# Kernel tuning notes

Measured on AMD Instinct MI355X. Metric: run time of the kernel, lower is better.

## Reference

```python
import jax, jax.numpy as jnp
import numpy as np

B, L, D = 8, 1024, 512
NB = 4              # num_blocks
DIN = 2 * D         # mamba expand=2
N = 16              # d_state
DTR = 32            # dt_rank = ceil(D/16)
DCONV = 4           # mamba depthwise conv kernel
FF = 2 * D          # ffn_expand=2
EPS = 1e-5


def setup_inputs() -> dict:
    key = jax.random.key(0)
    ks = iter(jax.random.split(key, 64))

    def rnd(shape, s=0.02):
        return jax.random.normal(next(ks), shape, jnp.float32) * s

    p = {}
    p["x"] = jax.random.normal(next(ks), (B, L, D), jnp.float32)
    # TemporalConvBlock (Conv1d D->D, k=3, pad=1, groups=1) + LayerNorm
    p["tconv_w"] = rnd((D, D, 3), 0.05)
    p["tconv_b"] = jnp.zeros((D,), jnp.float32)
    p["tnorm_w"] = jnp.ones((D,), jnp.float32)
    p["tnorm_b"] = jnp.zeros((D,), jnp.float32)
    # per-block params, stacked on leading NB axis
    p["ln1_w"] = jnp.ones((NB, D), jnp.float32)
    p["ln1_b"] = jnp.zeros((NB, D), jnp.float32)
    p["in_proj_w"] = rnd((NB, 2 * DIN, D))          # no bias (mamba default)
    p["conv_w"] = rnd((NB, DIN, 1, DCONV), 0.1)     # depthwise causal conv
    p["conv_b"] = jnp.zeros((NB, DIN), jnp.float32)
    p["x_proj_w"] = rnd((NB, DTR + 2 * N, DIN))     # no bias
    p["dt_proj_w"] = rnd((NB, DIN, DTR), 0.1)
    p["dt_proj_b"] = jnp.log(jnp.expm1(jnp.full((NB, DIN), 0.01, jnp.float32)))
    p["A_log"] = jnp.tile(jnp.log(jnp.arange(1, N + 1, dtype=jnp.float32))[None, None, :], (NB, DIN, 1))
    p["D_param"] = jnp.ones((NB, DIN), jnp.float32)
    p["out_proj_w"] = rnd((NB, D, DIN))             # no bias
    p["ln2_w"] = jnp.ones((NB, D), jnp.float32)
    p["ln2_b"] = jnp.zeros((NB, D), jnp.float32)
    p["ffn_w1"] = rnd((NB, FF, D))
    p["ffn_b1"] = jnp.zeros((NB, FF), jnp.float32)
    p["ffn_w2"] = rnd((NB, D, FF))
    p["ffn_b2"] = jnp.zeros((NB, D), jnp.float32)
    return p


def _ln(x, w, b):
    mu = jnp.mean(x, -1, keepdims=True)
    v = jnp.mean(jnp.square(x - mu), -1, keepdims=True)
    return (x - mu) * jax.lax.rsqrt(v + EPS) * w + b


def _selective_scan(u, dt, A, Bm, C, Dp):
    # u, dt: (B,L,DIN); A: (DIN,N); Bm, C: (B,L,N); Dp: (DIN,)
    def step(h, inp):
        u_t, dt_t, B_t, C_t = inp                      # (B,DIN),(B,DIN),(B,N),(B,N)
        dA = jnp.exp(dt_t[..., None] * A)              # (B,DIN,N)
        dBu = dt_t[..., None] * B_t[:, None, :] * u_t[..., None]
        h = dA * h + dBu
        y = jnp.einsum('bdn,bn->bd', h, C_t)
        return h, y

    h0 = jnp.zeros((u.shape[0], A.shape[0], A.shape[1]), u.dtype)
    xs = (u.swapaxes(0, 1), dt.swapaxes(0, 1), Bm.swapaxes(0, 1), C.swapaxes(0, 1))
    _, ys = jax.lax.scan(step, h0, xs)                 # ys: (L,B,DIN)
    return ys.swapaxes(0, 1) + u * Dp


def _mamba(x, in_w, cw, cb, xpw, dtw, dtb, A_log, Dp, ow):
    xz = jnp.einsum('bld,ed->ble', x, in_w)            # (B,L,2*DIN)
    u, z = jnp.split(xz, 2, axis=-1)
    # causal depthwise conv over time
    uc = u.swapaxes(1, 2)                              # (B,DIN,L)
    uc = jax.lax.conv_general_dilated(
        uc, cw, (1,), [(DCONV - 1, 0)],
        feature_group_count=DIN, dimension_numbers=('NCH', 'OIH', 'NCH'))
    uc = uc + cb[None, :, None]
    u = jax.nn.silu(uc.swapaxes(1, 2))                 # (B,L,DIN)
    xdb = jnp.einsum('bld,ed->ble', u, xpw)            # (B,L,DTR+2N)
    dtr, Bm, C = jnp.split(xdb, [DTR, DTR + N], axis=-1)
    dt = jax.nn.softplus(jnp.einsum('blr,dr->bld', dtr, dtw) + dtb)
    A = -jnp.exp(A_log)
    y = _selective_scan(u, dt, A, Bm, C, Dp)
    y = y * jax.nn.silu(z)
    return jnp.einsum('bld,ed->ble', y, ow)


def reference(x, tconv_w, tconv_b, tnorm_w, tnorm_b, ln1_w, ln1_b, in_proj_w,
              conv_w, conv_b, x_proj_w, dt_proj_w, dt_proj_b, A_log, D_param,
              out_proj_w, ln2_w, ln2_b, ffn_w1, ffn_b1, ffn_w2, ffn_b2):
    # TemporalConvBlock (dropout = identity in eval)
    hc = jax.lax.conv_general_dilated(
        x.swapaxes(1, 2), tconv_w, (1,), [(1, 1)],
        dimension_numbers=('NCH', 'OIH', 'NCH'))
    hc = (hc + tconv_b[None, :, None]).swapaxes(1, 2)
    h = _ln(hc + x, tnorm_w, tnorm_b)
    # stacked MambaWithFFN blocks
    for i in range(NB):
        h = h + _mamba(_ln(h, ln1_w[i], ln1_b[i]), in_proj_w[i], conv_w[i],
                       conv_b[i], x_proj_w[i], dt_proj_w[i], dt_proj_b[i],
                       A_log[i], D_param[i], out_proj_w[i])
        hn = _ln(h, ln2_w[i], ln2_b[i])
        ff = jax.nn.gelu(jnp.einsum('bld,fd->blf', hn, ffn_w1[i]) + ffn_b1[i],
                         approximate=False)
        h = h + jnp.einsum('blf,df->bld', ff, ffn_w2[i]) + ffn_b2[i]
    return h
```

## Files before the change

kernel.cpp:

```cpp
#include <hip/hip_runtime.h>
#include <hip/hip_bf16.h>
#include <math.h>

#define B_ 8
#define L_ 1024
#define D_ 512
#define NB_ 4
#define DIN_ 1024
#define NST_ 16
#define DTR_ 32
#define FF_ 1024
#define EPS_LN 1e-5f
#define M_ (B_ * L_)

#define SC_G 16
#define SC_C 32
#define SC_LEN (L_ / SC_C)

typedef __attribute__((ext_vector_type(8))) short short8;
typedef __attribute__((ext_vector_type(4))) float f32x4;

static __device__ __forceinline__ ushort f2bf(float f) {
  union { float f; unsigned u; } v; v.f = f;
  unsigned r = v.u + 0x7FFFu + ((v.u >> 16) & 1u);
  return (ushort)(r >> 16);
}
static __device__ __forceinline__ float bf2f(ushort u) {
  union { unsigned u; float f; } v; v.u = ((unsigned)u) << 16;
  return v.f;
}

template <int MODE, int EPI, int BN, int AF32, int OUTB>
__global__ __launch_bounds__(256) void mgemm_k(
    const void* __restrict__ Ap, const ushort* __restrict__ W,
    const float* __restrict__ bias, void* __restrict__ Cp,
    float* __restrict__ C2, int M, int N, int K, int lda, int ldc)
{
  constexpr int FN = BN / 32;
  __shared__ ushort As[128 * 32];
  __shared__ ushort Bs[BN * 32];
  const int tid = threadIdx.x;
  const int lane = tid & 63;
  const int wid = tid >> 6;
  const int wm = (wid >> 1) * 64;
  const int wn = (wid & 1) * (BN / 2);
  const int bm = blockIdx.y * 128;
  const int bn = blockIdx.x * BN;
  const int fr = lane & 15;
  const int kq = lane >> 4;

  f32x4 acc[4][FN];
#pragma unroll
  for (int i = 0; i < 4; ++i)
#pragma unroll
    for (int j = 0; j < FN; ++j) acc[i][j] = (f32x4)0.f;

  for (int k0 = 0; k0 < K; k0 += 32) {
#pragma unroll
    for (int it = 0; it < 2; ++it) {
      const int idx = tid + it * 256;
      const int row = idx >> 2;
      const int j = idx & 3;
      short8 s;
      if (AF32) {
        float4 v0, v1;
        if (MODE == 0) {
          const float* p = (const float*)Ap + (size_t)(bm + row) * lda + k0 + j * 8;
          v0 = *(const float4*)p; v1 = *(const float4*)(p + 4);
        } else {
          const int kk = k0 + j * 8;
          const int tap = kk >> 9;
          const int dcol = kk & 511;
          const int m = bm + row;
          const int l = (m & (L_ - 1)) + tap - 1;
          if (l >= 0 && l < L_) {
            const float* p = (const float*)Ap + (size_t)(m - (m & (L_ - 1)) + l) * D_ + dcol;
            v0 = *(const float4*)p; v1 = *(const float4*)(p + 4);
          } else {
            v0 = make_float4(0.f, 0.f, 0.f, 0.f); v1 = v0;
          }
        }
        s[0] = (short)f2bf(v0.x); s[1] = (short)f2bf(v0.y);
        s[2] = (short)f2bf(v0.z); s[3] = (short)f2bf(v0.w);
        s[4] = (short)f2bf(v1.x); s[5] = (short)f2bf(v1.y);
        s[6] = (short)f2bf(v1.z); s[7] = (short)f2bf(v1.w);
      } else {
        s = *(const short8*)((const ushort*)Ap + (size_t)(bm + row) * lda + k0 + j * 8);
      }
      *(short8*)&As[row * 32 + ((j ^ ((row >> 1) & 3)) << 3)] = s;
    }
#pragma unroll
    for (int it = 0; it < BN / 64; ++it) {
      const int idx = tid + it * 256;
      const int row = idx >> 2;
      const int j = idx & 3;
      short8 s = *(const short8*)(W + (size_t)(bn + row) * K + k0 + j * 8);
      *(short8*)&Bs[row * 32 + ((j ^ ((row >> 1) & 3)) << 3)] = s;
    }
    __syncthreads();
    short8 af[4], bfr[FN];
#pragma unroll
    for (int mi = 0; mi < 4; ++mi) {
      const int r = wm + mi * 16 + fr;
      af[mi] = *(const short8*)&As[r * 32 + ((kq ^ ((r >> 1) & 3)) << 3)];
    }
#pragma unroll
    for (int ni = 0; ni < FN; ++ni) {
      const int r = wn + ni * 16 + fr;
      bfr[ni] = *(const short8*)&Bs[r * 32 + ((kq ^ ((r >> 1) & 3)) << 3)];
    }
#pragma unroll
    for (int mi = 0; mi < 4; ++mi)
#pragma unroll
      for (int ni = 0; ni < FN; ++ni)
        acc[mi][ni] = __builtin_amdgcn_mfma_f32_16x16x32_bf16(
            af[mi], bfr[ni], acc[mi][ni], 0, 0, 0);
    __syncthreads();
  }

#pragma unroll
  for (int mi = 0; mi < 4; ++mi) {
#pragma unroll
    for (int ni = 0; ni < FN; ++ni) {
#pragma unroll
      for (int r = 0; r < 4; ++r) {
        const int gm = bm + wm + mi * 16 + (lane >> 4) * 4 + r;
        const int gn = bn + wn + ni * 16 + fr;
        float v = acc[mi][ni][r];
        if (EPI == 6) {
          if (gn < DIN_) {
            v += bias[gn];
            v = (v > 20.f) ? v : log1pf(__expf(v));
            ((float*)Cp)[(size_t)gm * DIN_ + gn] = v;
          } else if (gn < DIN_ + 2 * NST_) {
            C2[(size_t)gm * (2 * NST_) + (gn - DIN_)] = v;
          }
        } else {
          if (EPI == 1 || EPI == 2 || EPI == 3 || EPI == 5) v += bias[gn];
          if (EPI == 2) v = 0.5f * v * (1.f + erff(v * 0.70710678118654752f));
          if (EPI == 3) v = (v > 20.f) ? v : log1pf(__expf(v));
          if (OUTB) {
            ((ushort*)Cp)[(size_t)gm * ldc + gn] = f2bf(v);
          } else {
            float* pc = (float*)Cp + (size_t)gm * ldc + gn;
            if (EPI == 4 || EPI == 5) v += *pc;
            *pc = v;
          }
        }
      }
    }
  }
}

template <int INB, int OUTB>
__global__ __launch_bounds__(256) void ln_k(
    const void* __restrict__ inp, const float* __restrict__ res,
    const float* __restrict__ w, const float* __restrict__ b,
    void* __restrict__ outp)
{
  const int row = blockIdx.x;
  const int t = threadIdx.x;
  float v0, v1;
  if (INB) {
    const ushort* p = (const ushort*)inp + (size_t)row * D_;
    v0 = bf2f(p[t]); v1 = bf2f(p[t + 256]);
  } else {
    const float* p = (const float*)inp + (size_t)row * D_;
    v0 = p[t]; v1 = p[t + 256];
  }
  if (res) {
    const float* r = res + (size_t)row * D_;
    v0 += r[t]; v1 += r[t + 256];
  }
  float s = v0 + v1;
  float sq = v0 * v0 + v1 * v1;
#pragma unroll
  for (int m = 1; m < 64; m <<= 1) {
    s += __shfl_xor(s, m, 64);
    sq += __shfl_xor(sq, m, 64);
  }
  __shared__ float ss[4], qq[4];
  const int wid = t >> 6;
  if ((t & 63) == 0) { ss[wid] = s; qq[wid] = sq; }
  __syncthreads();
  s = ss[0] + ss[1] + ss[2] + ss[3];
  sq = qq[0] + qq[1] + qq[2] + qq[3];
  const float mu = s * (1.f / (float)D_);
  const float var = sq * (1.f / (float)D_) - mu * mu;
  const float rs = rsqrtf(var + EPS_LN);
  const float o0 = (v0 - mu) * rs * w[t] + b[t];
  const float o1 = (v1 - mu) * rs * w[t + 256] + b[t + 256];
  if (OUTB) {
    ushort* o = (ushort*)outp + (size_t)row * D_;
    o[t] = f2bf(o0); o[t + 256] = f2bf(o1);
  } else {
    float* o = (float*)outp + (size_t)row * D_;
    o[t] = o0; o[t + 256] = o1;
  }
}

__global__ __launch_bounds__(256) void dwconv_k(
    const ushort* __restrict__ xz, const float* __restrict__ cw,
    const float* __restrict__ cb, ushort* __restrict__ u)
{
  const int idx = blockIdx.x * 256 + threadIdx.x;
  const int c8 = idx & (DIN_ / 8 - 1);
  const int bl = idx >> 7;
  const int l = bl & (L_ - 1);
  const int b0 = bl - l;
  const int c0 = c8 * 8;
  float s[8], w[8][4];
#pragma unroll
  for (int j = 0; j < 8; ++j) {
    s[j] = cb[c0 + j];
    const float4 wv = *(const float4*)(cw + (c0 + j) * 4);
    w[j][0] = wv.x; w[j][1] = wv.y; w[j][2] = wv.z; w[j][3] = wv.w;
  }
#pragma unroll
  for (int k = 0; k < 4; ++k) {
    const int ll = l + k - 3;
    if (ll >= 0) {
      const short8 v = *(const short8*)(xz + (size_t)(b0 + ll) * (2 * DIN_) + c0);
#pragma unroll
      for (int j = 0; j < 8; ++j)
        s[j] = fmaf(bf2f((ushort)v[j]), w[j][k], s[j]);
    }
  }
  short8 o;
#pragma unroll
  for (int j = 0; j < 8; ++j) {
    const float t = s[j] / (1.f + __expf(-s[j]));
    o[j] = (short)f2bf(t);
  }
  *(short8*)(u + (size_t)idx * 8) = o;
}

template <bool FAST>
static __device__ __forceinline__ void dAcalc(float dtv, float A0,
                                              const float* A, float* dA)
{
  if (FAST) {
    const float e = __expf(dtv * A0);
    dA[0] = e;
#pragma unroll
    for (int n = 1; n < 16; ++n) dA[n] = dA[n - 1] * e;
  } else {
#pragma unroll
    for (int n = 0; n < 16; ++n) dA[n] = __expf(dtv * A[n]);
  }
}

template <bool FAST>
static __device__ __forceinline__ void scan_run(
    const float* __restrict__ dt, ushort* __restrict__ u,
    const float* __restrict__ BC, const ushort* __restrict__ xz,
    const float* __restrict__ A_log,
    const float* A, const float A0, const float Dpd,
    float (*Hs)[SC_G][NST_ + 1], float (*Ss)[SC_G],
    const int tid, const int g, const int c, const int d0, const int d,
    const size_t base)
{
  const int l0 = c * SC_LEN;
  float h[16];
#pragma unroll
  for (int n = 0; n < 16; ++n) h[n] = 0.f;
  float S = 0.f;

  {
    size_t row = base + l0;
    float dtv = dt[row * DIN_ + d];
    float uv = bf2f(u[row * DIN_ + d]);
    float Bv[16];
    *(float4*)&Bv[0]  = *(const float4*)(BC + row * 32);
    *(float4*)&Bv[4]  = *(const float4*)(BC + row * 32 + 4);
    *(float4*)&Bv[8]  = *(const float4*)(BC + row * 32 + 8);
    *(float4*)&Bv[12] = *(const float4*)(BC + row * 32 + 12);
    for (int i = 0; i < SC_LEN; ++i) {
      float ndt = 0.f, nu = 0.f;
      float NBv[16];
      if (i + 1 < SC_LEN) {
        const size_t nrow = row + 1;
        ndt = dt[nrow * DIN_ + d];
        nu = bf2f(u[nrow * DIN_ + d]);
        *(float4*)&NBv[0]  = *(const float4*)(BC + nrow * 32);
        *(float4*)&NBv[4]  = *(const float4*)(BC + nrow * 32 + 4);
        *(float4*)&NBv[8]  = *(const float4*)(BC + nrow * 32 + 8);
        *(float4*)&NBv[12] = *(const float4*)(BC + nrow * 32 + 12);
      }
      S += dtv;
      const float du = dtv * uv;
      float dA[16];
      dAcalc<FAST>(dtv, A0, A, dA);
#pragma unroll
      for (int n = 0; n < 16; ++n)
        h[n] = fmaf(dA[n], h[n], du * Bv[n]);
      dtv = ndt; uv = nu;
#pragma unroll
      for (int n = 0; n < 16; ++n) Bv[n] = NBv[n];
      row += 1;
    }
  }
#pragma unroll
  for (int n = 0; n < 16; ++n) Hs[c][g][n] = h[n];
  Ss[c][g] = S;
  __syncthreads();

  if (tid < SC_G * NST_) {
    const int gg = tid >> 4;
    const int n2 = tid & 15;
    const float An = -expf(A_log[(d0 + gg) * NST_ + n2]);
    float hin = 0.f;
#pragma unroll
    for (int cc = 0; cc < SC_C; ++cc) {
      const float tmp = Hs[cc][gg][n2];
      const float P = __expf(An * Ss[cc][gg]);
      Hs[cc][gg][n2] = hin;
      hin = tmp + P * hin;
    }
  }
  __syncthreads();

#pragma unroll
  for (int n = 0; n < 16; ++n) h[n] = Hs[c][g][n];
  {
    size_t row = base + l0;
    float dtv = dt[row * DIN_ + d];
    float uv = bf2f(u[row * DIN_ + d]);
    float zv = bf2f(xz[row * (2 * DIN_) + DIN_ + d]);
    float Bv[16], Cv[16];
    *(float4*)&Bv[0]  = *(const float4*)(BC + row * 32);
    *(float4*)&Bv[4]  = *(const float4*)(BC + row * 32 + 4);
    *(float4*)&Bv[8]  = *(const float4*)(BC + row * 32 + 8);
    *(float4*)&Bv[12] = *(const float4*)(BC + row * 32 + 12);
    *(float4*)&Cv[0]  = *(const float4*)(BC + row * 32 + 16);
    *(float4*)&Cv[4]  = *(const float4*)(BC + row * 32 + 20);
    *(float4*)&Cv[8]  = *(const float4*)(BC + row * 32 + 24);
    *(float4*)&Cv[12] = *(const float4*)(BC + row * 32 + 28);
    for (int i = 0; i < SC_LEN; ++i) {
      float ndt = 0.f, nu = 0.f, nz = 0.f;
      float NBv[16], NCv[16];
      if (i + 1 < SC_LEN) {
        const size_t nrow = row + 1;
        ndt = dt[nrow * DIN_ + d];
        nu = bf2f(u[nrow * DIN_ + d]);
        nz = bf2f(xz[nrow * (2 * DIN_) + DIN_ + d]);
        *(float4*)&NBv[0]  = *(const float4*)(BC + nrow * 32);
        *(float4*)&NBv[4]  = *(const float4*)(BC + nrow * 32 + 4);
        *(float4*)&NBv[8]  = *(const float4*)(BC + nrow * 32 + 8);
        *(float4*)&NBv[12] = *(const float4*)(BC + nrow * 32 + 12);
        *(float4*)&NCv[0]  = *(const float4*)(BC + nrow * 32 + 16);
        *(float4*)&NCv[4]  = *(const float4*)(BC + nrow * 32 + 20);
        *(float4*)&NCv[8]  = *(const float4*)(BC + nrow * 32 + 24);
        *(float4*)&NCv[12] = *(const float4*)(BC + nrow * 32 + 28);
      }
      const float du = dtv * uv;
      float y = uv * Dpd;
      float dA[16];
      dAcalc<FAST>(dtv, A0, A, dA);
#pragma unroll
      for (int n = 0; n < 16; ++n) {
        h[n] = fmaf(dA[n], h[n], du * Bv[n]);
        y = fmaf(h[n], Cv[n], y);
      }
      y *= zv / (1.f + __expf(-zv));
      u[row * DIN_ + d] = f2bf(y);
      dtv = ndt; uv = nu; zv = nz;
#pragma unroll
      for (int n = 0; n < 16; ++n) { Bv[n] = NBv[n]; Cv[n] = NCv[n]; }
      row += 1;
    }
  }
}

__global__ __launch_bounds__(512) void scan5_k(
    const float* __restrict__ dt, ushort* u,
    const float* __restrict__ BC, const ushort* __restrict__ xz,
    const float* __restrict__ A_log, const float* __restrict__ Dp)
{
  const int tid = threadIdx.x;
  const int g = tid & (SC_G - 1);
  const int c = tid >> 4;
  const int b = blockIdx.x >> 6;
  const int d0 = (blockIdx.x & 63) * SC_G;
  const int d = d0 + g;

  __shared__ float Hs[SC_C][SC_G][NST_ + 1];
  __shared__ float Ss[SC_C][SC_G];
  __shared__ int slow;
  if (tid == 0) slow = 0;
  __syncthreads();

  float A[16];
#pragma unroll
  for (int n = 0; n < 16; ++n) A[n] = -expf(A_log[d * NST_ + n]);
  const float A0 = A[0];
  bool myfast = true;
#pragma unroll
  for (int n = 1; n < 16; ++n)
    myfast = myfast && (fabsf(A[n] - (float)(n + 1) * A0) <= 1e-3f * fabsf(A[n]));
  if (!myfast) slow = 1;
  __syncthreads();
  const float Dpd = Dp[d];
  const size_t base = (size_t)b * L_;

  if (slow == 0)
    scan_run<true>(dt, u, BC, xz, A_log, A, A0, Dpd, Hs, Ss, tid, g, c, d0, d, base);
  else
    scan_run<false>(dt, u, BC, xz, A_log, A, A0, Dpd, Hs, Ss, tid, g, c, d0, d, base);
}

__global__ __launch_bounds__(256) void cvt_k(const float* __restrict__ in,
                                             ushort* __restrict__ out, int n8)
{
  const int i = blockIdx.x * 256 + threadIdx.x;
  if (i >= n8) return;
  const float4 a = *(const float4*)(in + (size_t)i * 8);
  const float4 b = *(const float4*)(in + (size_t)i * 8 + 4);
  short8 s;
  s[0] = (short)f2bf(a.x); s[1] = (short)f2bf(a.y);
  s[2] = (short)f2bf(a.z); s[3] = (short)f2bf(a.w);
  s[4] = (short)f2bf(b.x); s[5] = (short)f2bf(b.y);
  s[6] = (short)f2bf(b.z); s[7] = (short)f2bf(b.w);
  *(short8*)(out + (size_t)i * 8) = s;
}

__global__ __launch_bounds__(256) void twt_k(const float* __restrict__ in,
                                             ushort* __restrict__ out)
{
  const int i = blockIdx.x * 256 + threadIdx.x;
  if (i >= D_ * D_ * 3) return;
  const int o = i / (D_ * 3);
  const int rem = i - o * (D_ * 3);
  const int d = rem / 3;
  const int tap = rem - d * 3;
  out[(size_t)o * (D_ * 3) + tap * D_ + d] = f2bf(in[i]);
}

__global__ __launch_bounds__(256) void xpT_k(const float* __restrict__ xpw,
                                             ushort* __restrict__ out)
{
  const int i = blockIdx.x * 256 + threadIdx.x;
  if (i >= DIN_ * DTR_) return;
  const int k = i >> 5;
  const int r = i & 31;
  out[i] = f2bf(xpw[(size_t)r * DIN_ + k]);
}

__global__ __launch_bounds__(256) void pack_k(const float* __restrict__ wc,
                                              const float* __restrict__ xpw,
                                              ushort* __restrict__ wbig)
{
  const int i = blockIdx.x * 256 + threadIdx.x;
  if (i >= 1088 * 1024) return;
  const int r = i >> 10;
  const int k = i & 1023;
  float v;
  if (r < 1024) v = wc[i];
  else if (r < 1056) v = xpw[(size_t)(DTR_ + r - 1024) * DIN_ + k];
  else v = 0.f;
  wbig[i] = f2bf(v);
}

extern "C" void kernel_launch(void* const* d_in, const int* in_sizes, int n_in,
                              void* d_out, int out_size, void* d_ws, size_t ws_size,
                              hipStream_t stream)
{
  const float* x         = (const float*)d_in[0];
  const float* tconv_w   = (const float*)d_in[1];
  const float* tconv_b   = (const float*)d_in[2];
  const float* tnorm_w   = (const float*)d_in[3];
  const float* tnorm_b   = (const float*)d_in[4];
  const float* ln1_w     = (const float*)d_in[5];
  const float* ln1_b     = (const float*)d_in[6];
  const float* in_proj_w = (const float*)d_in[7];
  const float* conv_w    = (const float*)d_in[8];
  const float* conv_b    = (const float*)d_in[9];
  const float* x_proj_w  = (const float*)d_in[10];
  const float* dt_proj_w = (const float*)d_in[11];
  const float* dt_proj_b = (const float*)d_in[12];
  const float* A_log     = (const float*)d_in[13];
  const float* D_param   = (const float*)d_in[14];
  const float* out_proj_w= (const float*)d_in[15];
  const float* ln2_w     = (const float*)d_in[16];
  const float* ln2_b     = (const float*)d_in[17];
  const float* ffn_w1    = (const float*)d_in[18];
  const float* ffn_b1    = (const float*)d_in[19];
  const float* ffn_w2    = (const float*)d_in[20];
  const float* ffn_b2    = (const float*)d_in[21];

  float* h = (float*)d_out;

  char* p = (char*)d_ws;
  ushort* wTT  = (ushort*)p; p += (size_t)512 * 1536 * 2;
  ushort* wIP  = (ushort*)p; p += (size_t)4 * 2048 * 512 * 2;
  ushort* wOP  = (ushort*)p; p += (size_t)4 * 512 * 1024 * 2;
  ushort* wF1  = (ushort*)p; p += (size_t)4 * 1024 * 512 * 2;
  ushort* wF2  = (ushort*)p; p += (size_t)4 * 512 * 1024 * 2;
  ushort* xpwT = (ushort*)p; p += (size_t)4 * 1024 * 32 * 2;
  ushort* wBig = (ushort*)p; p += (size_t)4 * 1088 * 1024 * 2;
  float*  wcT  = (float*)p;  p += (size_t)1024 * 1024 * 4;
  ushort* xin  = (ushort*)p; p += (size_t)M_ * 512 * 2;
  ushort* xzb  = (ushort*)p; p += (size_t)M_ * 2048 * 2;
  ushort* ubuf = (ushort*)p; p += (size_t)M_ * 1024 * 2;
  float*  bc   = (float*)p;  p += (size_t)M_ * 32 * 4;
  float*  dtb  = (float*)p;  p += (size_t)M_ * 1024 * 4;
  ushort* ff   = (ushort*)p; p += (size_t)M_ * 1024 * 2;

  const dim3 blk(256);

  cvt_k<<<dim3(4 * 2048 * 512 / 8 / 256), blk, 0, stream>>>(in_proj_w, wIP, 4 * 2048 * 512 / 8);
  cvt_k<<<dim3(4 * 512 * 1024 / 8 / 256), blk, 0, stream>>>(out_proj_w, wOP, 4 * 512 * 1024 / 8);
  cvt_k<<<dim3(4 * 1024 * 512 / 8 / 256), blk, 0, stream>>>(ffn_w1, wF1, 4 * 1024 * 512 / 8);
  cvt_k<<<dim3(4 * 512 * 1024 / 8 / 256), blk, 0, stream>>>(ffn_w2, wF2, 4 * 512 * 1024 / 8);
  twt_k<<<dim3((D_ * D_ * 3 + 255) / 256), blk, 0, stream>>>(tconv_w, wTT);
  for (int i = 0; i < NB_; ++i)
    xpT_k<<<dim3(DIN_ * DTR_ / 256), blk, 0, stream>>>(
        x_proj_w + (size_t)i * 64 * DIN_, xpwT + (size_t)i * DIN_ * DTR_);
  for (int i = 0; i < NB_; ++i) {
    mgemm_k<0, 0, 128, 1, 0><<<dim3(8, 8), blk, 0, stream>>>(
        dt_proj_w + (size_t)i * DIN_ * DTR_, xpwT + (size_t)i * DIN_ * DTR_,
        nullptr, wcT, nullptr, 1024, 1024, 32, 32, 1024);
    pack_k<<<dim3(1088 * 1024 / 256), blk, 0, stream>>>(
        wcT, x_proj_w + (size_t)i * 64 * DIN_, wBig + (size_t)i * 1088 * 1024);
  }

  mgemm_k<1, 1, 64, 1, 1><<<dim3(8, 64), blk, 0, stream>>>(
      x, wTT, tconv_b, xin, nullptr, M_, 512, 1536, 0, 512);
  ln_k<1, 0><<<dim3(M_), blk, 0, stream>>>(xin, x, tnorm_w, tnorm_b, h);

  for (int i = 0; i < NB_; ++i) {
    ln_k<0, 1><<<dim3(M_), blk, 0, stream>>>(h, nullptr, ln1_w + i * D_, ln1_b + i * D_, xin);
    mgemm_k<0, 0, 128, 0, 1><<<dim3(16, 64), blk, 0, stream>>>(
        xin, wIP + (size_t)i * 2048 * 512, nullptr, xzb, nullptr,
        M_, 2048, 512, 512, 2048);
    dwconv_k<<<dim3(M_ * DIN_ / 8 / 256), blk, 0, stream>>>(
        xzb, conv_w + (size_t)i * DIN_ * 4, conv_b + (size_t)i * DIN_, ubuf);
    mgemm_k<0, 6, 64, 0, 0><<<dim3(17, 64), blk, 0, stream>>>(
        ubuf, wBig + (size_t)i * 1088 * 1024, dt_proj_b + (size_t)i * DIN_,
        dtb, bc, M_, 1088, 1024, 1024, 1024);
    scan5_k<<<dim3(B_ * (DIN_ / SC_G)), dim3(512), 0, stream>>>(
        dtb, ubuf, bc, xzb, A_log + (size_t)i * DIN_ * NST_, D_param + (size_t)i * DIN_);
    mgemm_k<0, 4, 64, 0, 0><<<dim3(8, 64), blk, 0, stream>>>(
        ubuf, wOP + (size_t)i * 512 * 1024, nullptr, h, nullptr,
        M_, 512, 1024, 1024, 512);
    ln_k<0, 1><<<dim3(M_), blk, 0, stream>>>(h, nullptr, ln2_w + i * D_, ln2_b + i * D_, xin);
    mgemm_k<0, 2, 64, 0, 1><<<dim3(16, 64), blk, 0, stream>>>(
        xin, wF1 + (size_t)i * 1024 * 512, ffn_b1 + (size_t)i * FF_, ff, nullptr,
        M_, 1024, 512, 512, 1024);
    mgemm_k<0, 5, 64, 0, 0><<<dim3(8, 64), blk, 0, stream>>>(
        ff, wF2 + (size_t)i * 512 * 1024, ffn_b2 + (size_t)i * D_, h, nullptr,
        M_, 512, 1024, 1024, 512);
  }
}
```

Measured before the change: 1.474 ms.

## Add bf16 GEMM kernel using direct global-to-LDS loads with BK=64 tiles

Introduces mgemm2_k, a bf16-input GEMM that loads A and W tiles straight into LDS via global_load_lds with an XOR swizzle and a K-step of 64, instead of staging through registers. All per-block GEMMs (in_proj, x_proj/dt, out_proj, FFN1, FFN2) move to it with 128-wide N tiles and per-call BM choices. The packed x_proj weight is padded from 1088 to 1152 rows to fit the 128 N tile, at the cost of some wasted compute. Softplus uses fast __logf, and the old kernel is trimmed to the fp32-input cases only.

Result: faster. 1.390 ms (-5.6%).

```diff
diff --git a/kernel.cpp b/kernel.cpp
--- a/kernel.cpp
+++ b/kernel.cpp
@@ -30,11 +30,118 @@
   return v.f;
 }
 
-template <int MODE, int EPI, int BN, int AF32, int OUTB>
-__global__ __launch_bounds__(256) void mgemm_k(
-    const void* __restrict__ Ap, const ushort* __restrict__ W,
+static __device__ __forceinline__ void gll16(const void* g, void* l) {
+  __builtin_amdgcn_global_load_lds(
+      (const __attribute__((address_space(1))) void*)g,
+      (__attribute__((address_space(3))) void*)l, 16, 0, 0);
+}
+
+template <int BM, int EPI, int OUTB>
+__global__ __launch_bounds__(256) void mgemm2_k(
+    const ushort* __restrict__ A, const ushort* __restrict__ W,
     const float* __restrict__ bias, void* __restrict__ Cp,
     float* __restrict__ C2, int M, int N, int K, int lda, int ldc)
+{
+  constexpr int MI = BM / 32;
+  __shared__ ushort As[BM * 64];
+  __shared__ ushort Bs[128 * 64];
+  const int tid = threadIdx.x;
+  const int lane = tid & 63;
+  const int wid = tid >> 6;
+  const int wm = (wid >> 1) * (BM / 2);
+  const int wn = (wid & 1) * 64;
+  const int bm = blockIdx.y * BM;
+  const int bn = blockIdx.x * 128;
+  const int fr = lane & 15;
+  const int kq = lane >> 4;
+
+  f32x4 acc[MI][4];
+#pragma unroll
+  for (int i = 0; i < MI; ++i)
+#pragma unroll
+    for (int j = 0; j < 4; ++j) acc[i][j] = (f32x4)0.f;
+
+  for (int k0 = 0; k0 < K; k0 += 64) {
+#pragma unroll
+    for (int it = 0; it < BM / 32; ++it) {
+      const int sb = it * 4096 + wid * 1024 + lane * 16;
+      const int row = sb >> 7;
+      const int js = (sb >> 4) & 7;
+      const int j2 = js ^ (row & 7);
+      gll16(A + (size_t)(bm + row) * lda + k0 + j2 * 8,
+            (char*)As + it * 4096 + wid * 1024);
+    }
+#pragma unroll
+    for (int it = 0; it < 4; ++it) {
+      const int sb = it * 4096 + wid * 1024 + lane * 16;
+      const int row = sb >> 7;
+      const int js = (sb >> 4) & 7;
+      const int j2 = js ^ (row & 7);
+      gll16(W + (size_t)(bn + row) * K + k0 + j2 * 8,
+            (char*)Bs + it * 4096 + wid * 1024);
+    }
+    __syncthreads();
+#pragma unroll
+    for (int kk = 0; kk < 2; ++kk) {
+      short8 af[MI], bf[4];
+#pragma unroll
+      for (int mi = 0; mi < MI; ++mi) {
+        const int r = wm + mi * 16 + fr;
+        af[mi] = *(const short8*)&As[r * 64 + ((((kk << 2) + kq) ^ (r & 7)) << 3)];
+      }
+#pragma unroll
+      for (int ni = 0; ni < 4; ++ni) {
+        const int r = wn + ni * 16 + fr;
+        bf[ni] = *(const short8*)&Bs[r * 64 + ((((kk << 2) + kq) ^ (r & 7)) << 3)];
+      }
+#pragma unroll
+      for (int mi = 0; mi < MI; ++mi)
+#pragma unroll
+        for (int ni = 0; ni < 4; ++ni)
+          acc[mi][ni] = __builtin_amdgcn_mfma_f32_16x16x32_bf16(
+              af[mi], bf[ni], acc[mi][ni], 0, 0, 0);
+    }
+    __syncthreads();
+  }
+
+#pragma unroll
+  for (int mi = 0; mi < MI; ++mi) {
+#pragma unroll
+    for (int ni = 0; ni < 4; ++ni) {
+#pragma unroll
+      for (int r = 0; r < 4; ++r) {
+        const int gm = bm + wm + mi * 16 + (lane >> 4) * 4 + r;
+        const int gn = bn + wn + ni * 16 + fr;
+        float v = acc[mi][ni][r];
+        if (EPI == 6) {
+          if (gn < DIN_) {
+            v += bias[gn];
+            v = (v > 20.f) ? v : __logf(1.f + __expf(v));
+            ((float*)Cp)[(size_t)gm * DIN_ + gn] = v;
+          } else if (gn < DIN_ + 2 * NST_) {
+            C2[(size_t)gm * (2 * NST_) + (gn - DIN_)] = v;
+          }
+        } else {
+          if (EPI == 2 || EPI == 5) v += bias[gn];
+          if (EPI == 2) v = 0.5f * v * (1.f + erff(v * 0.70710678118654752f));
+          if (OUTB) {
+            ((ushort*)Cp)[(size_t)gm * ldc + gn] = f2bf(v);
+          } else {
+            float* pc = (float*)Cp + (size_t)gm * ldc + gn;
+            if (EPI == 4 || EPI == 5) v += *pc;
+            *pc = v;
+          }
+        }
+      }
+    }
+  }
+}
+
+template <int MODE, int EPI, int BN, int OUTB>
+__global__ __launch_bounds__(256) void mgemm_k(
+    const float* __restrict__ Ap, const ushort* __restrict__ W,
+    const float* __restrict__ bias, void* __restrict__ Cp,
+    int M, int N, int K, int lda, int ldc)
 {
   constexpr int FN = BN / 32;
   __shared__ ushort As[128 * 32];
@@ -62,31 +169,27 @@
       const int row = idx >> 2;
       const int j = idx & 3;
       short8 s;
-      if (AF32) {
-        float4 v0, v1;
-        if (MODE == 0) {
-          const float* p = (const float*)Ap + (size_t)(bm + row) * lda + k0 + j * 8;
+      float4 v0, v1;
+      if (MODE == 0) {
+        const float* p = Ap + (size_t)(bm + row) * lda + k0 + j * 8;
+        v0 = *(const float4*)p; v1 = *(const float4*)(p + 4);
+      } else {
+        const int kk = k0 + j * 8;
+        const int tap = kk >> 9;
+        const int dcol = kk & 511;
+        const int m = bm + row;
+        const int l = (m & (L_ - 1)) + tap - 1;
+        if (l >= 0 && l < L_) {
+          const float* p = Ap + (size_t)(m - (m & (L_ - 1)) + l) * D_ + dcol;
           v0 = *(const float4*)p; v1 = *(const float4*)(p + 4);
         } else {
-          const int kk = k0 + j * 8;
-          const int tap = kk >> 9;
-          const int dcol = kk & 511;
-          const int m = bm + row;
-          const int l = (m & (L_ - 1)) + tap - 1;
-          if (l >= 0 && l < L_) {
-            const float* p = (const float*)Ap + (size_t)(m - (m & (L_ - 1)) + l) * D_ + dcol;
-            v0 = *(const float4*)p; v1 = *(const float4*)(p + 4);
-          } else {
-            v0 = make_float4(0.f, 0.f, 0.f, 0.f); v1 = v0;
-          }
+          v0 = make_float4(0.f, 0.f, 0.f, 0.f); v1 = v0;
         }
-        s[0] = (short)f2bf(v0.x); s[1] = (short)f2bf(v0.y);
-        s[2] = (short)f2bf(v0.z); s[3] = (short)f2bf(v0.w);
-        s[4] = (short)f2bf(v1.x); s[5] = (short)f2bf(v1.y);
-        s[6] = (short)f2bf(v1.z); s[7] = (short)f2bf(v1.w);
-      } else {
-        s = *(const short8*)((const ushort*)Ap + (size_t)(bm + row) * lda + k0 + j * 8);
-      }
+      }
+      s[0] = (short)f2bf(v0.x); s[1] = (short)f2bf(v0.y);
+      s[2] = (short)f2bf(v0.z); s[3] = (short)f2bf(v0.w);
+      s[4] = (short)f2bf(v1.x); s[5] = (short)f2bf(v1.y);
+      s[6] = (short)f2bf(v1.z); s[7] = (short)f2bf(v1.w);
       *(short8*)&As[row * 32 + ((j ^ ((row >> 1) & 3)) << 3)] = s;
     }
 #pragma unroll
@@ -127,26 +230,9 @@
         const int gm = bm + wm + mi * 16 + (lane >> 4) * 4 + r;
         const int gn = bn + wn + ni * 16 + fr;
         float v = acc[mi][ni][r];
-        if (EPI == 6) {
-          if (gn < DIN_) {
-            v += bias[gn];
-            v = (v > 20.f) ? v : log1pf(__expf(v));
-            ((float*)Cp)[(size_t)gm * DIN_ + gn] = v;
-          } else if (gn < DIN_ + 2 * NST_) {
-            C2[(size_t)gm * (2 * NST_) + (gn - DIN_)] = v;
-          }
-        } else {
-          if (EPI == 1 || EPI == 2 || EPI == 3 || EPI == 5) v += bias[gn];
-          if (EPI == 2) v = 0.5f * v * (1.f + erff(v * 0.70710678118654752f));
-          if (EPI == 3) v = (v > 20.f) ? v : log1pf(__expf(v));
-          if (OUTB) {
-            ((ushort*)Cp)[(size_t)gm * ldc + gn] = f2bf(v);
-          } else {
-            float* pc = (float*)Cp + (size_t)gm * ldc + gn;
-            if (EPI == 4 || EPI == 5) v += *pc;
-            *pc = v;
-          }
-        }
+        if (EPI == 1) v += bias[gn];
+        if (OUTB) ((ushort*)Cp)[(size_t)gm * ldc + gn] = f2bf(v);
+        else ((float*)Cp)[(size_t)gm * ldc + gn] = v;
       }
     }
   }
@@ -451,7 +537,7 @@
                                               ushort* __restrict__ wbig)
 {
   const int i = blockIdx.x * 256 + threadIdx.x;
-  if (i >= 1088 * 1024) return;
+  if (i >= 1152 * 1024) return;
   const int r = i >> 10;
   const int k = i & 1023;
   float v;
@@ -497,7 +583,7 @@
   ushort* wF1  = (ushort*)p; p += (size_t)4 * 1024 * 512 * 2;
   ushort* wF2  = (ushort*)p; p += (size_t)4 * 512 * 1024 * 2;
   ushort* xpwT = (ushort*)p; p += (size_t)4 * 1024 * 32 * 2;
-  ushort* wBig = (ushort*)p; p += (size_t)4 * 1088 * 1024 * 2;
+  ushort* wBig = (ushort*)p; p += (size_t)4 * 1152 * 1024 * 2;
   float*  wcT  = (float*)p;  p += (size_t)1024 * 1024 * 4;
   ushort* xin  = (ushort*)p; p += (size_t)M_ * 512 * 2;
   ushort* xzb  = (ushort*)p; p += (size_t)M_ * 2048 * 2;
@@ -517,37 +603,37 @@
     xpT_k<<<dim3(DIN_ * DTR_ / 256), blk, 0, stream>>>(
         x_proj_w + (size_t)i * 64 * DIN_, xpwT + (size_t)i * DIN_ * DTR_);
   for (int i = 0; i < NB_; ++i) {
-    mgemm_k<0, 0, 128, 1, 0><<<dim3(8, 8), blk, 0, stream>>>(
+    mgemm_k<0, 0, 128, 0><<<dim3(8, 8), blk, 0, stream>>>(
         dt_proj_w + (size_t)i * DIN_ * DTR_, xpwT + (size_t)i * DIN_ * DTR_,
-        nullptr, wcT, nullptr, 1024, 1024, 32, 32, 1024);
-    pack_k<<<dim3(1088 * 1024 / 256), blk, 0, stream>>>(
-        wcT, x_proj_w + (size_t)i * 64 * DIN_, wBig + (size_t)i * 1088 * 1024);
-  }
-
-  mgemm_k<1, 1, 64, 1, 1><<<dim3(8, 64), blk, 0, stream>>>(
-      x, wTT, tconv_b, xin, nullptr, M_, 512, 1536, 0, 512);
+        nullptr, wcT, 1024, 1024, 32, 32, 1024);
+    pack_k<<<dim3(1152 * 1024 / 256), blk, 0, stream>>>(
+        wcT, x_proj_w + (size_t)i * 64 * DIN_, wBig + (size_t)i * 1152 * 1024);
+  }
+
+  mgemm_k<1, 1, 64, 1><<<dim3(8, 64), blk, 0, stream>>>(
+      x, wTT, tconv_b, xin, M_, 512, 1536, 0, 512);
   ln_k<1, 0><<<dim3(M_), blk, 0, stream>>>(xin, x, tnorm_w, tnorm_b, h);
 
   for (int i = 0; i < NB_; ++i) {
     ln_k<0, 1><<<dim3(M_), blk, 0, stream>>>(h, nullptr, ln1_w + i * D_, ln1_b + i * D_, xin);
-    mgemm_k<0, 0, 128, 0, 1><<<dim3(16, 64), blk, 0, stream>>>(
+    mgemm2_k<128, 0, 1><<<dim3(16, 64), blk, 0, stream>>>(
         xin, wIP + (size_t)i * 2048 * 512, nullptr, xzb, nullptr,
         M_, 2048, 512, 512, 2048);
     dwconv_k<<<dim3(M_ * DIN_ / 8 / 256), blk, 0, stream>>>(
         xzb, conv_w + (size_t)i * DIN_ * 4, conv_b + (size_t)i * DIN_, ubuf);
-    mgemm_k<0, 6, 64, 0, 0><<<dim3(17, 64), blk, 0, stream>>>(
-        ubuf, wBig + (size_t)i * 1088 * 1024, dt_proj_b + (size_t)i * DIN_,
-        dtb, bc, M_, 1088, 1024, 1024, 1024);
+    mgemm2_k<128, 6, 0><<<dim3(9, 64), blk, 0, stream>>>(
+        ubuf, wBig + (size_t)i * 1152 * 1024, dt_proj_b + (size_t)i * DIN_,
+        dtb, bc, M_, 1152, 1024, 1024, 1024);
     scan5_k<<<dim3(B_ * (DIN_ / SC_G)), dim3(512), 0, stream>>>(
         dtb, ubuf, bc, xzb, A_log + (size_t)i * DIN_ * NST_, D_param + (size_t)i * DIN_);
-    mgemm_k<0, 4, 64, 0, 0><<<dim3(8, 64), blk, 0, stream>>>(
+    mgemm2_k<64, 4, 0><<<dim3(4, 128), blk, 0, stream>>>(
         ubuf, wOP + (size_t)i * 512 * 1024, nullptr, h, nullptr,
         M_, 512, 1024, 1024, 512);
     ln_k<0, 1><<<dim3(M_), blk, 0, stream>>>(h, nullptr, ln2_w + i * D_, ln2_b + i * D_, xin);
-    mgemm_k<0, 2, 64, 0, 1><<<dim3(16, 64), blk, 0, stream>>>(
+    mgemm2_k<128, 2, 1><<<dim3(8, 64), blk, 0, stream>>>(
         xin, wF1 + (size_t)i * 1024 * 512, ffn_b1 + (size_t)i * FF_, ff, nullptr,
         M_, 1024, 512, 512, 1024);
-    mgemm_k<0, 5, 64, 0, 0><<<dim3(8, 64), blk, 0, stream>>>(
+    mgemm2_k<64, 5, 0><<<dim3(4, 128), blk, 0, stream>>>(
         ff, wF2 + (size_t)i * 512 * 1024, ffn_b2 + (size_t)i * D_, h, nullptr,
         M_, 512, 1024, 1024, 512);
   }
```
